# Optimization experiments

Measured on AMD Instinct MI355X. Metric: run time of the kernel, lower is better.

## Reference

```python
import jax, jax.numpy as jnp
import numpy as np

B = 16384   # batch (agents x parallel envs)
IN = 12     # input_dim
H = 64      # hidden_dim -> 2H = 128
OUT = 25    # output_dim (forced by x[:,0:5]..x[:,20:25] slicing)


def setup_inputs() -> dict:
    key = jax.random.key(0)
    ks = jax.random.split(key, 24)
    n = lambda k, s: jax.random.normal(k, s, dtype=jnp.float32)
    s = 0.1  # scale params to keep SiLU/softmax in a sane range
    return {
        "x": n(ks[0], (B, IN)),
        "na": 4,
        # mlp_in: Linear(IN, 2H) + SiLU
        "W_in": n(ks[1], (2 * H, IN)) * s, "b_in": n(ks[2], (2 * H,)) * s,
        # first attention (2H)
        "Aq4": n(ks[3], (2 * H, 2 * H)) * s, "Bq4": n(ks[4], (2 * H,)) * s,
        "Ak4": n(ks[5], (2 * H, 2 * H)) * s, "Bk4": n(ks[6], (2 * H,)) * s,
        "Av4": n(ks[7], (2 * H, 2 * H)) * s, "Bv4": n(ks[8], (2 * H,)) * s,
        # mlp_hidden_4: Linear(2H, H) + SiLU
        "W_h": n(ks[9], (H, 2 * H)) * s, "b_h": n(ks[10], (H,)) * s,
        # second attention (H)
        "Aq7": n(ks[11], (H, H)) * s, "Bq7": n(ks[12], (H,)) * s,
        "Ak7": n(ks[13], (H, H)) * s, "Bk7": n(ks[14], (H,)) * s,
        "Av7": n(ks[15], (H, H)) * s, "Bv7": n(ks[16], (H,)) * s,
        # mlp_out: Linear(H, OUT) + SiLU
        "W_out": n(ks[17], (OUT, H)) * s, "b_out": n(ks[18], (OUT,)) * s,
    }


def _attn(h, Aq, Bq, Ak, Bk, Av, Bv):
    # h: [B, D]; torch does bmm(A, x^T)+B with x of shape [B,1,D] -> seq-len-1
    # attention, i.e. scores are an outer product q k^T of shape [B, D, D].
    q = jax.nn.silu(h @ Aq.T + Bq)                      # [B, D]
    k = jax.nn.silu(h @ Ak.T + Bk)                      # [B, D]
    v = jax.nn.silu(h @ Av.T + Bv)                      # [B, D]
    a = jax.nn.softmax(q[:, :, None] * k[:, None, :], axis=2)  # [B, D, D]
    return jax.nn.silu(jnp.einsum("bij,bj->bi", a, v))  # [B, D]


def reference(x, na, W_in, b_in, Aq4, Bq4, Ak4, Bk4, Av4, Bv4,
              W_h, b_h, Aq7, Bq7, Ak7, Bk7, Av7, Bv7, W_out, b_out):
    h = jax.nn.silu(x @ W_in.T + b_in)                  # [B, 2H]
    h = _attn(h, Aq4, Bq4, Ak4, Bk4, Av4, Bv4)          # [B, 2H]
    h = jax.nn.silu(h @ W_h.T + b_h)                    # [B, H]
    h = _attn(h, Aq7, Bq7, Ak7, Bk7, Av7, Bv7)          # [B, H]
    y = jax.nn.silu(h @ W_out.T + b_out)                # [B, 25]

    # block-diagonal quadratic-form assembly (l=2, kron with ones(1,2))
    M11 = jnp.sum(y[:, 0:5] ** 2, axis=1)               # [B]
    M12 = jnp.sum(y[:, 5:10] ** 2, axis=1)
    M21 = jnp.sum(y[:, 10:15] ** 2, axis=1)
    M22 = jnp.sum(y[:, 15:20] ** 2, axis=1)
    Mpp = jnp.sum(y[:, 20:25] ** 2, axis=1)             # [B]
    q = y[:, :4]                                        # [B, 4] = [q0,q1,q2,q3]
    # M = [[diag(M11), diag(M12)],[diag(M21), diag(M22)]] (each 2x2 diag)
    quad = (M11 * (q[:, 0] ** 2 + q[:, 1] ** 2)
            + (M12 + M21) * (q[:, 0] * q[:, 2] + q[:, 1] * q[:, 3])
            + M22 * (q[:, 2] ** 2 + q[:, 3] ** 2))
    return (quad + Mpp)[:, None]                        # [B, 1]
```

## Files before the change

### kernel.cpp

```cpp
#include <hip/hip_runtime.h>

#define RPW 4
#define WAVES 4
#define RPB (RPW * WAVES)
#define NM 14

using short8 = __attribute__((ext_vector_type(8))) short;
using f32x4  = __attribute__((ext_vector_type(4))) float;

#define LOG2E 1.4426950408889634f

static __device__ __forceinline__ float ex2(float x) { return __builtin_amdgcn_exp2f(x); }
static __device__ __forceinline__ float rcpf_(float x) { return __builtin_amdgcn_rcpf(x); }
static __device__ __forceinline__ float silu_(float x) {
    return x * rcpf_(1.0f + ex2(-x * LOG2E));
}
static __device__ __forceinline__ unsigned short bfhi(float x) {
    return (unsigned short)(__float_as_uint(x) >> 16);
}
static __device__ __forceinline__ unsigned short bfrn(float x) {
    unsigned u = __float_as_uint(x);
    return (unsigned short)((u + 0x7fffu + ((u >> 16) & 1u)) >> 16);
}
static __device__ __forceinline__ float bf2f(unsigned short h) {
    return __uint_as_float(((unsigned)h) << 16);
}

template <int CTRL>
static __device__ __forceinline__ float dpp_rot(float v) {
    return __uint_as_float(
        __builtin_amdgcn_update_dpp(0u, __float_as_uint(v), CTRL, 0xF, 0xF, true));
}
static __device__ __forceinline__ float rsum16(float v) {
    v += dpp_rot<0x128>(v);
    v += dpp_rot<0x124>(v);
    v += dpp_rot<0x122>(v);
    v += dpp_rot<0x121>(v);
    return v;
}

__constant__ float c_invfact[15] = {
    1.f, 1.f, 0.5f, 1.f/6, 1.f/24, 1.f/120, 1.f/720, 1.f/5040, 1.f/40320,
    1.f/362880, 1.f/3628800, 1.f/39916800, 1.f/479001600,
    1.f/6227020800.f, 1.f/87178291200.f};

template <int O, int I>
__device__ __forceinline__ void tr(const float* __restrict__ s, float* __restrict__ d,
                                   int t0, int stride) {
    for (int idx = t0; idx < O * I; idx += stride) {
        int o = idx / I, in = idx - o * I;
        d[in * O + o] = s[idx];
    }
}
template <int N>
__device__ __forceinline__ void cvt(const float* __restrict__ s,
                                    unsigned short* __restrict__ hi,
                                    unsigned short* __restrict__ lo,
                                    int t0, int stride) {
    for (int i = t0; i < N; i += stride) {
        float a = s[i];
        unsigned short h = bfhi(a);
        float r = a - bf2f(h);
        hi[i] = h;
        lo[i] = bfhi(r);
    }
}

__global__ void tweights(const float* __restrict__ s0, const float* __restrict__ s1,
                         const float* __restrict__ s2, const float* __restrict__ s3,
                         const float* __restrict__ s4, const float* __restrict__ s5,
                         const float* __restrict__ s6, const float* __restrict__ s7,
                         const float* __restrict__ s8, float* __restrict__ ws) {
    const int stride = gridDim.x * blockDim.x;
    const int t0 = blockIdx.x * blockDim.x + threadIdx.x;
    tr<128, 12>(s0, ws + 0, t0, stride);
    unsigned short* u4 = (unsigned short*)(ws + 1536);
    cvt<128 * 128>(s1, u4 + 0,     u4 + 16384, t0, stride);
    cvt<128 * 128>(s2, u4 + 32768, u4 + 49152, t0, stride);
    cvt<128 * 128>(s3, u4 + 65536, u4 + 81920, t0, stride);
    unsigned short* wh = (unsigned short*)(ws + 50688);
    cvt<64 * 128>(s4, wh + 0, wh + 8192, t0, stride);
    unsigned short* u7 = (unsigned short*)(ws + 58880);
    cvt<64 * 64>(s5, u7 + 0,     u7 + 4096,  t0, stride);
    cvt<64 * 64>(s6, u7 + 8192,  u7 + 12288, t0, stride);
    cvt<64 * 64>(s7, u7 + 16384, u7 + 20480, t0, stride);
    tr<25, 64>(s8, ws + 71168, t0, stride);
}

__global__ __launch_bounds__(256, 4) void fused_net(
    const float* __restrict__ x, const float* __restrict__ ws,
    const float* __restrict__ b_in,
    const float* __restrict__ Bq4, const float* __restrict__ Bk4, const float* __restrict__ Bv4,
    const float* __restrict__ b_h,
    const float* __restrict__ Bq7, const float* __restrict__ Bk7, const float* __restrict__ Bv7,
    const float* __restrict__ b_out,
    float* __restrict__ out) {
    __shared__ __align__(16) unsigned short hAhi[16][136], hAlo[16][136];
    __shared__ __align__(16) unsigned short h2hi[16][80],  h2lo[16][80];
    __shared__ __align__(16) float sQ[16][132];
    __shared__ __align__(16) unsigned short sKVb[16][132][2];
    __shared__ __align__(16) float h3T[WAVES][64][RPW];
    __shared__ __align__(16) float sXT[WAVES][12][RPW];
    __shared__ __align__(16) float sY[WAVES][RPW][26];

    const int tid = threadIdx.x;
    const int w = tid >> 6;
    const int l = tid & 63;
    const int row0 = blockIdx.x * RPB + w * RPW;
    const int m16 = l & 15, quad = l >> 4;
    const int g = l & 15, r = l >> 4;
    const int R = w * RPW + r;

    const float* WinT  = ws + 0;
    const float* WoutT = ws + 71168;

    if (l < 12 * RPW) {
        float v = x[row0 * 12 + l];
        int rr = l / 12, in = l - rr * 12;
        sXT[w][in][rr] = v;
    }

    {
        float2 bb = *(const float2*)&b_in[2 * l];
        float a0[RPW], a1[RPW];
        #pragma unroll
        for (int rr = 0; rr < RPW; rr++) { a0[rr] = bb.x; a1[rr] = bb.y; }
        #pragma unroll
        for (int in = 0; in < 12; in++) {
            float2 wv = *(const float2*)&WinT[in * 128 + 2 * l];
            float4 xr = *(const float4*)&sXT[w][in][0];
            a0[0] = fmaf(xr.x, wv.x, a0[0]); a1[0] = fmaf(xr.x, wv.y, a1[0]);
            a0[1] = fmaf(xr.y, wv.x, a0[1]); a1[1] = fmaf(xr.y, wv.y, a1[1]);
            a0[2] = fmaf(xr.z, wv.x, a0[2]); a1[2] = fmaf(xr.z, wv.y, a1[2]);
            a0[3] = fmaf(xr.w, wv.x, a0[3]); a1[3] = fmaf(xr.w, wv.y, a1[3]);
        }
        #pragma unroll
        for (int rr = 0; rr < RPW; rr++) {
            float h0 = silu_(a0[rr]), h1 = silu_(a1[rr]);
            unsigned short h0h = bfhi(h0), h1h = bfhi(h1);
            float r0 = h0 - bf2f(h0h), r1 = h1 - bf2f(h1h);
            *(unsigned*)&hAhi[w * 4 + rr][2 * l] = (unsigned)h0h | ((unsigned)h1h << 16);
            *(unsigned*)&hAlo[w * 4 + rr][2 * l] = (unsigned)bfhi(r0) | ((unsigned)bfhi(r1) << 16);
        }
    }
    __syncthreads();

    {
        short8 Ah[4], Al[4];
        #pragma unroll
        for (int kt = 0; kt < 4; kt++) {
            Ah[kt] = *(const short8*)&hAhi[m16][kt * 32 + quad * 8];
            Al[kt] = *(const short8*)&hAlo[m16][kt * 32 + quad * 8];
        }
        const unsigned short* u4 = (const unsigned short*)(ws + 1536);
        #pragma unroll
        for (int t = 0; t < 6; t++) {
            const int nt = w * 6 + t;
            const int mat = nt >> 3;
            const int n = (nt & 7) * 16 + m16;
            const float* bp = (mat == 0) ? Bq4 : (mat == 1) ? Bk4 : Bv4;
            float b = bp[n];
            f32x4 acc = {b, b, b, b};
            const unsigned short* Bh = u4 + mat * 32768 + n * 128;
            const unsigned short* Bl = Bh + 16384;
            #pragma unroll
            for (int kt = 0; kt < 4; kt++) {
                short8 bh = *(const short8*)&Bh[kt * 32 + quad * 8];
                short8 bl = *(const short8*)&Bl[kt * 32 + quad * 8];
                acc = __builtin_amdgcn_mfma_f32_16x16x32_bf16(Ah[kt], bh, acc, 0, 0, 0);
                acc = __builtin_amdgcn_mfma_f32_16x16x32_bf16(Ah[kt], bl, acc, 0, 0, 0);
                acc = __builtin_amdgcn_mfma_f32_16x16x32_bf16(Al[kt], bh, acc, 0, 0, 0);
            }
            #pragma unroll
            for (int reg = 0; reg < 4; reg++) {
                int row = quad * 4 + reg;
                float val = silu_(acc[reg]);
                if (mat == 0)      sQ[row][n] = val;
                else if (mat == 1) sKVb[row][n][0] = bfrn(val);
                else               sKVb[row][n][1] = bfrn(val);
            }
        }
    }
    __syncthreads();

    {
        float dmom[NM];
        float nmom[NM + 1];
        #pragma unroll
        for (int m = 0; m < NM; m++) dmom[m] = 0.f;
        #pragma unroll
        for (int m = 0; m <= NM; m++) nmom[m] = 0.f;
        uint4 u0 = *(const uint4*)&sKVb[R][g * 8][0];
        uint4 u1 = *(const uint4*)&sKVb[R][g * 8 + 4][0];
        unsigned us[8] = {u0.x, u0.y, u0.z, u0.w, u1.x, u1.y, u1.z, u1.w};
        #pragma unroll
        for (int jj = 0; jj < 8; jj++) {
            unsigned u = us[jj];
            float kf = __uint_as_float(u << 16);
            float vf = __uint_as_float(u & 0xffff0000u);
            nmom[0] += vf;
            float p = kf;
            dmom[0] += p; nmom[1] = fmaf(vf, p, nmom[1]);
            #pragma unroll
            for (int m = 1; m < NM; m++) {
                p *= kf;
                dmom[m] += p;
                nmom[m + 1] = fmaf(vf, p, nmom[m + 1]);
            }
        }
        #pragma unroll
        for (int m = 0; m < NM; m++) dmom[m] = rsum16(dmom[m]);
        #pragma unroll
        for (int m = 0; m <= NM; m++) nmom[m] = rsum16(nmom[m]);
        float cd[NM + 1], cn[NM + 1];
        cd[0] = 128.f; cn[0] = nmom[0];
        #pragma unroll
        for (int m = 1; m <= NM; m++) {
            cd[m] = dmom[m - 1] * c_invfact[m];
            cn[m] = nmom[m] * c_invfact[m];
        }
        float4 qa = *(const float4*)&sQ[R][g * 8];
        float4 qb = *(const float4*)&sQ[R][g * 8 + 4];
        float qs[8] = {qa.x, qa.y, qa.z, qa.w, qb.x, qb.y, qb.z, qb.w};
        unsigned hiw[4], low[4];
        #pragma unroll
        for (int i = 0; i < 8; i++) {
            float t = qs[i];
            float d = cd[NM], nn = cn[NM];
            #pragma unroll
            for (int m = NM - 1; m >= 0; m--) {
                d = fmaf(d, t, cd[m]);
                nn = fmaf(nn, t, cn[m]);
            }
            float o = silu_(nn * rcpf_(d));
            unsigned short oh = bfhi(o);
            unsigned short olo = bfhi(o - bf2f(oh));
            if (i & 1) { hiw[i >> 1] |= ((unsigned)oh) << 16; low[i >> 1] |= ((unsigned)olo) << 16; }
            else       { hiw[i >> 1] = oh; low[i >> 1] = olo; }
        }
        *(uint4*)&hAhi[R][g * 8] = make_uint4(hiw[0], hiw[1], hiw[2], hiw[3]);
        *(uint4*)&hAlo[R][g * 8] = make_uint4(low[0], low[1], low[2], low[3]);
    }
    __syncthreads();

    {
        short8 Ah[4], Al[4];
        #pragma unroll
        for (int kt = 0; kt < 4; kt++) {
            Ah[kt] = *(const short8*)&hAhi[m16][kt * 32 + quad * 8];
            Al[kt] = *(const short8*)&hAlo[m16][kt * 32 + quad * 8];
        }
        const unsigned short* whh = (const unsigned short*)(ws + 50688);
        const unsigned short* whl = whh + 8192;
        const int n = w * 16 + m16;
        float b = b_h[n];
        f32x4 acc = {b, b, b, b};
        #pragma unroll
        for (int kt = 0; kt < 4; kt++) {
            short8 bh = *(const short8*)&whh[n * 128 + kt * 32 + quad * 8];
            short8 bl = *(const short8*)&whl[n * 128 + kt * 32 + quad * 8];
            acc = __builtin_amdgcn_mfma_f32_16x16x32_bf16(Ah[kt], bh, acc, 0, 0, 0);
            acc = __builtin_amdgcn_mfma_f32_16x16x32_bf16(Ah[kt], bl, acc, 0, 0, 0);
            acc = __builtin_amdgcn_mfma_f32_16x16x32_bf16(Al[kt], bh, acc, 0, 0, 0);
        }
        #pragma unroll
        for (int reg = 0; reg < 4; reg++) {
            int row = quad * 4 + reg;
            float hv = silu_(acc[reg]);
            unsigned short hh = bfhi(hv);
            h2hi[row][n] = hh;
            h2lo[row][n] = bfhi(hv - bf2f(hh));
        }
    }
    __syncthreads();

    {
        short8 Ah[2], Al[2];
        #pragma unroll
        for (int kt = 0; kt < 2; kt++) {
            Ah[kt] = *(const short8*)&h2hi[m16][kt * 32 + quad * 8];
            Al[kt] = *(const short8*)&h2lo[m16][kt * 32 + quad * 8];
        }
        const unsigned short* u7 = (const unsigned short*)(ws + 58880);
        #pragma unroll
        for (int t = 0; t < 3; t++) {
            const int nt = w * 3 + t;
            const int mat = nt >> 2;
            const int n = (nt & 3) * 16 + m16;
            const float* bp = (mat == 0) ? Bq7 : (mat == 1) ? Bk7 : Bv7;
            float b = bp[n];
            f32x4 acc = {b, b, b, b};
            const unsigned short* Bh = u7 + mat * 8192 + n * 64;
            const unsigned short* Bl = Bh + 4096;
            #pragma unroll
            for (int kt = 0; kt < 2; kt++) {
                short8 bh = *(const short8*)&Bh[kt * 32 + quad * 8];
                short8 bl = *(const short8*)&Bl[kt * 32 + quad * 8];
                acc = __builtin_amdgcn_mfma_f32_16x16x32_bf16(Ah[kt], bh, acc, 0, 0, 0);
                acc = __builtin_amdgcn_mfma_f32_16x16x32_bf16(Ah[kt], bl, acc, 0, 0, 0);
                acc = __builtin_amdgcn_mfma_f32_16x16x32_bf16(Al[kt], bh, acc, 0, 0, 0);
            }
            #pragma unroll
            for (int reg = 0; reg < 4; reg++) {
                int row = quad * 4 + reg;
                float val = silu_(acc[reg]);
                if (mat == 0)      sQ[row][n] = val;
                else if (mat == 1) sKVb[row][n][0] = bfrn(val);
                else               sKVb[row][n][1] = bfrn(val);
            }
        }
    }
    __syncthreads();

    {
        float dmom[NM];
        float nmom[NM + 1];
        #pragma unroll
        for (int m = 0; m < NM; m++) dmom[m] = 0.f;
        #pragma unroll
        for (int m = 0; m <= NM; m++) nmom[m] = 0.f;
        uint4 u0 = *(const uint4*)&sKVb[R][g * 4][0];
        unsigned us[4] = {u0.x, u0.y, u0.z, u0.w};
        #pragma unroll
        for (int jj = 0; jj < 4; jj++) {
            unsigned u = us[jj];
            float kf = __uint_as_float(u << 16);
            float vf = __uint_as_float(u & 0xffff0000u);
            nmom[0] += vf;
            float p = kf;
            dmom[0] += p; nmom[1] = fmaf(vf, p, nmom[1]);
            #pragma unroll
            for (int m = 1; m < NM; m++) {
                p *= kf;
                dmom[m] += p;
                nmom[m + 1] = fmaf(vf, p, nmom[m + 1]);
            }
        }
        #pragma unroll
        for (int m = 0; m < NM; m++) dmom[m] = rsum16(dmom[m]);
        #pragma unroll
        for (int m = 0; m <= NM; m++) nmom[m] = rsum16(nmom[m]);
        float cd[NM + 1], cn[NM + 1];
        cd[0] = 64.f; cn[0] = nmom[0];
        #pragma unroll
        for (int m = 1; m <= NM; m++) {
            cd[m] = dmom[m - 1] * c_invfact[m];
            cn[m] = nmom[m] * c_invfact[m];
        }
        float4 qa = *(const float4*)&sQ[R][g * 4];
        float qs[4] = {qa.x, qa.y, qa.z, qa.w};
        #pragma unroll
        for (int i = 0; i < 4; i++) {
            float t = qs[i];
            float d = cd[NM], nn = cn[NM];
            #pragma unroll
            for (int m = NM - 1; m >= 0; m--) {
                d = fmaf(d, t, cd[m]);
                nn = fmaf(nn, t, cn[m]);
            }
            h3T[w][g * 4 + i][r] = silu_(nn * rcpf_(d));
        }
    }

    {
        const int o = l & 31;
        const int half = l >> 5;
        const int oc = (o < 25) ? o : 0;
        float y[RPW];
        float bb = (half == 0) ? b_out[oc] : 0.f;
        #pragma unroll
        for (int rr = 0; rr < RPW; rr++) y[rr] = bb;
        const int in0 = half * 32;
        #pragma unroll 4
        for (int i = 0; i < 32; i++) {
            int in = in0 + i;
            float wv = WoutT[in * 25 + oc];
            float4 xr = *(const float4*)&h3T[w][in][0];
            y[0] = fmaf(xr.x, wv, y[0]);
            y[1] = fmaf(xr.y, wv, y[1]);
            y[2] = fmaf(xr.z, wv, y[2]);
            y[3] = fmaf(xr.w, wv, y[3]);
        }
        #pragma unroll
        for (int rr = 0; rr < RPW; rr++) {
            float full = y[rr] + __shfl_xor(y[rr], 32, 64);
            if (l < 25) sY[w][rr][l] = silu_(full);
        }
    }

    if (l < RPW) {
        const int rr = l;
        float y[25];
        #pragma unroll
        for (int c = 0; c < 25; c++) y[c] = sY[w][rr][c];
        float M11 = 0.f, M12 = 0.f, M21 = 0.f, M22 = 0.f, Mpp = 0.f;
        #pragma unroll
        for (int c = 0; c < 5; c++) {
            M11 = fmaf(y[c], y[c], M11);
            M12 = fmaf(y[5 + c], y[5 + c], M12);
            M21 = fmaf(y[10 + c], y[10 + c], M21);
            M22 = fmaf(y[15 + c], y[15 + c], M22);
            Mpp = fmaf(y[20 + c], y[20 + c], Mpp);
        }
        float quad = M11 * (y[0] * y[0] + y[1] * y[1])
                   + (M12 + M21) * (y[0] * y[2] + y[1] * y[3])
                   + M22 * (y[2] * y[2] + y[3] * y[3]);
        out[row0 + rr] = quad + Mpp;
    }
}

extern "C" void kernel_launch(void* const* d_in, const int* in_sizes, int n_in,
                              void* d_out, int out_size, void* d_ws, size_t ws_size,
                              hipStream_t stream) {
    const float* x    = (const float*)d_in[0];
    const float* W_in = (const float*)d_in[2];
    const float* b_in = (const float*)d_in[3];
    const float* Aq4  = (const float*)d_in[4];
    const float* Bq4  = (const float*)d_in[5];
    const float* Ak4  = (const float*)d_in[6];
    const float* Bk4  = (const float*)d_in[7];
    const float* Av4  = (const float*)d_in[8];
    const float* Bv4  = (const float*)d_in[9];
    const float* W_h  = (const float*)d_in[10];
    const float* b_h  = (const float*)d_in[11];
    const float* Aq7  = (const float*)d_in[12];
    const float* Bq7  = (const float*)d_in[13];
    const float* Ak7  = (const float*)d_in[14];
    const float* Bk7  = (const float*)d_in[15];
    const float* Av7  = (const float*)d_in[16];
    const float* Bv7  = (const float*)d_in[17];
    const float* Wout = (const float*)d_in[18];
    const float* bout = (const float*)d_in[19];
    float* ws = (float*)d_ws;

    tweights<<<256, 256, 0, stream>>>(W_in, Aq4, Ak4, Av4, W_h, Aq7, Ak7, Av7, Wout, ws);

    const int B = in_sizes[0] / 12;
    const int grid = B / RPB;
    fused_net<<<grid, 256, 0, stream>>>(x, ws, b_in, Bq4, Bk4, Bv4,
                                        b_h, Bq7, Bk7, Bv7, bout, (float*)d_out);
}
```

Measured before the change: 137.1 us.

## Pre-swizzle weights into MFMA fragment order and prefetch B-fragments ahead of use

```diff
diff --git a/kernel.cpp b/kernel.cpp
--- a/kernel.cpp
+++ b/kernel.cpp
@@ -52,17 +52,23 @@
         d[in * O + o] = s[idx];
     }
 }
-template <int N>
-__device__ __forceinline__ void cvt(const float* __restrict__ s,
-                                    unsigned short* __restrict__ hi,
-                                    unsigned short* __restrict__ lo,
-                                    int t0, int stride) {
-    for (int i = t0; i < N; i += stride) {
-        float a = s[i];
-        unsigned short h = bfhi(a);
-        float r = a - bf2f(h);
-        hi[i] = h;
-        lo[i] = bfhi(r);
+
+template <int TILES, int KTS, int K>
+__device__ __forceinline__ void frag_cvt(const float* __restrict__ A,
+                                         unsigned short* __restrict__ dst,
+                                         int t0, int stride) {
+    const int total = TILES * KTS * 2 * 512;
+    for (int idx = t0; idx < total; idx += stride) {
+        int e = idx & 7;
+        int lane = (idx >> 3) & 63;
+        int h = (idx >> 9) & 1;
+        int kt = (idx >> 10) % KTS;
+        int tile = (idx >> 10) / KTS;
+        int row = tile * 16 + (lane & 15);
+        int col = kt * 32 + (lane >> 4) * 8 + e;
+        float a = A[row * K + col];
+        unsigned short hi = bfhi(a);
+        dst[idx] = h ? bfhi(a - bf2f(hi)) : hi;
     }
 }
 
@@ -70,21 +76,20 @@
                          const float* __restrict__ s2, const float* __restrict__ s3,
                          const float* __restrict__ s4, const float* __restrict__ s5,
                          const float* __restrict__ s6, const float* __restrict__ s7,
-                         const float* __restrict__ s8, float* __restrict__ ws) {
+                         float* __restrict__ ws) {
     const int stride = gridDim.x * blockDim.x;
     const int t0 = blockIdx.x * blockDim.x + threadIdx.x;
     tr<128, 12>(s0, ws + 0, t0, stride);
     unsigned short* u4 = (unsigned short*)(ws + 1536);
-    cvt<128 * 128>(s1, u4 + 0,     u4 + 16384, t0, stride);
-    cvt<128 * 128>(s2, u4 + 32768, u4 + 49152, t0, stride);
-    cvt<128 * 128>(s3, u4 + 65536, u4 + 81920, t0, stride);
+    frag_cvt<8, 4, 128>(s1, u4 + 0,     t0, stride);
+    frag_cvt<8, 4, 128>(s2, u4 + 32768, t0, stride);
+    frag_cvt<8, 4, 128>(s3, u4 + 65536, t0, stride);
     unsigned short* wh = (unsigned short*)(ws + 50688);
-    cvt<64 * 128>(s4, wh + 0, wh + 8192, t0, stride);
+    frag_cvt<4, 4, 128>(s4, wh, t0, stride);
     unsigned short* u7 = (unsigned short*)(ws + 58880);
-    cvt<64 * 64>(s5, u7 + 0,     u7 + 4096,  t0, stride);
-    cvt<64 * 64>(s6, u7 + 8192,  u7 + 12288, t0, stride);
-    cvt<64 * 64>(s7, u7 + 16384, u7 + 20480, t0, stride);
-    tr<25, 64>(s8, ws + 71168, t0, stride);
+    frag_cvt<4, 2, 64>(s5, u7 + 0,     t0, stride);
+    frag_cvt<4, 2, 64>(s6, u7 + 8192,  t0, stride);
+    frag_cvt<4, 2, 64>(s7, u7 + 16384, t0, stride);
 }
 
 __global__ __launch_bounds__(256, 4) void fused_net(
@@ -93,7 +98,7 @@
     const float* __restrict__ Bq4, const float* __restrict__ Bk4, const float* __restrict__ Bv4,
     const float* __restrict__ b_h,
     const float* __restrict__ Bq7, const float* __restrict__ Bk7, const float* __restrict__ Bv7,
-    const float* __restrict__ b_out,
+    const float* __restrict__ Wout, const float* __restrict__ b_out,
     float* __restrict__ out) {
     __shared__ __align__(16) unsigned short hAhi[16][136], hAlo[16][136];
     __shared__ __align__(16) unsigned short h2hi[16][80],  h2lo[16][80];
@@ -111,8 +116,27 @@
     const int g = l & 15, r = l >> 4;
     const int R = w * RPW + r;
 
-    const float* WinT  = ws + 0;
-    const float* WoutT = ws + 71168;
+    const float* WinT = ws + 0;
+
+    float bias4[6];
+    #pragma unroll
+    for (int t = 0; t < 6; t++) {
+        const int nt = w * 6 + t;
+        const int mat = nt >> 3;
+        const int n = (nt & 7) * 16 + m16;
+        const float* bp = (mat == 0) ? Bq4 : (mat == 1) ? Bk4 : Bv4;
+        bias4[t] = bp[n];
+    }
+    float biasH = b_h[w * 16 + m16];
+    float bias7[3];
+    #pragma unroll
+    for (int t = 0; t < 3; t++) {
+        const int nt = w * 3 + t;
+        const int mat = nt >> 2;
+        const int n = (nt & 3) * 16 + m16;
+        const float* bp = (mat == 0) ? Bq7 : (mat == 1) ? Bk7 : Bv7;
+        bias7[t] = bp[n];
+    }
 
     if (l < 12 * RPW) {
         float v = x[row0 * 12 + l];
@@ -152,37 +176,57 @@
             Ah[kt] = *(const short8*)&hAhi[m16][kt * 32 + quad * 8];
             Al[kt] = *(const short8*)&hAlo[m16][kt * 32 + quad * 8];
         }
-        const unsigned short* u4 = (const unsigned short*)(ws + 1536);
+        const unsigned short* F4 = (const unsigned short*)(ws + 1536);
+        short8 cb[4][2], nb[4][2];
+        auto ldt = [&](int t, short8 fr[4][2]) {
+            const int nt = w * 6 + t;
+            const int mat = nt >> 3, tile = nt & 7;
+            const unsigned short* bp = F4 + mat * 32768 + tile * 4096 + l * 8;
+            #pragma unroll
+            for (int kt = 0; kt < 4; kt++) {
+                fr[kt][0] = *(const short8*)(bp + kt * 1024);
+                fr[kt][1] = *(const short8*)(bp + kt * 1024 + 512);
+            }
+        };
+        ldt(0, cb);
         #pragma unroll
         for (int t = 0; t < 6; t++) {
+            if (t < 5) ldt(t + 1, nb);
+            f32x4 acc0 = {0.f, 0.f, 0.f, 0.f};
+            f32x4 acc1 = {0.f, 0.f, 0.f, 0.f};
+            #pragma unroll
+            for (int kt = 0; kt < 4; kt++) {
+                acc0 = __builtin_amdgcn_mfma_f32_16x16x32_bf16(Ah[kt], cb[kt][0], acc0, 0, 0, 0);
+                acc1 = __builtin_amdgcn_mfma_f32_16x16x32_bf16(Ah[kt], cb[kt][1], acc1, 0, 0, 0);
+                acc1 = __builtin_amdgcn_mfma_f32_16x16x32_bf16(Al[kt], cb[kt][0], acc1, 0, 0, 0);
+            }
             const int nt = w * 6 + t;
             const int mat = nt >> 3;
             const int n = (nt & 7) * 16 + m16;
-            const float* bp = (mat == 0) ? Bq4 : (mat == 1) ? Bk4 : Bv4;
-            float b = bp[n];
-            f32x4 acc = {b, b, b, b};
-            const unsigned short* Bh = u4 + mat * 32768 + n * 128;
-            const unsigned short* Bl = Bh + 16384;
-            #pragma unroll
-            for (int kt = 0; kt < 4; kt++) {
-                short8 bh = *(const short8*)&Bh[kt * 32 + quad * 8];
-                short8 bl = *(const short8*)&Bl[kt * 32 + quad * 8];
-                acc = __builtin_amdgcn_mfma_f32_16x16x32_bf16(Ah[kt], bh, acc, 0, 0, 0);
-                acc = __builtin_amdgcn_mfma_f32_16x16x32_bf16(Ah[kt], bl, acc, 0, 0, 0);
-                acc = __builtin_amdgcn_mfma_f32_16x16x32_bf16(Al[kt], bh, acc, 0, 0, 0);
-            }
+            const float b = bias4[t];
             #pragma unroll
             for (int reg = 0; reg < 4; reg++) {
                 int row = quad * 4 + reg;
-                float val = silu_(acc[reg]);
+                float val = silu_(b + acc0[reg] + acc1[reg]);
                 if (mat == 0)      sQ[row][n] = val;
                 else if (mat == 1) sKVb[row][n][0] = bfrn(val);
                 else               sKVb[row][n][1] = bfrn(val);
             }
+            #pragma unroll
+            for (int kt = 0; kt < 4; kt++) { cb[kt][0] = nb[kt][0]; cb[kt][1] = nb[kt][1]; }
         }
     }
     __syncthreads();
 
+    short8 whf[4][2];
+    {
+        const unsigned short* bp = (const unsigned short*)(ws + 50688) + w * 4096 + l * 8;
+        #pragma unroll
+        for (int kt = 0; kt < 4; kt++) {
+            whf[kt][0] = *(const short8*)(bp + kt * 1024);
+            whf[kt][1] = *(const short8*)(bp + kt * 1024 + 512);
+        }
+    }
     {
         float dmom[NM];
         float nmom[NM + 1];
@@ -243,6 +287,21 @@
     }
     __syncthreads();
 
+    short8 u7f[3][2][2];
+    {
+        const unsigned short* U7 = (const unsigned short*)(ws + 58880);
+        #pragma unroll
+        for (int t = 0; t < 3; t++) {
+            const int nt = w * 3 + t;
+            const int mat = nt >> 2, tile = nt & 3;
+            const unsigned short* bp = U7 + mat * 8192 + tile * 2048 + l * 8;
+            #pragma unroll
+            for (int kt = 0; kt < 2; kt++) {
+                u7f[t][kt][0] = *(const short8*)(bp + kt * 1024);
+                u7f[t][kt][1] = *(const short8*)(bp + kt * 1024 + 512);
+            }
+        }
+    }
     {
         short8 Ah[4], Al[4];
         #pragma unroll
@@ -250,23 +309,19 @@
             Ah[kt] = *(const short8*)&hAhi[m16][kt * 32 + quad * 8];
             Al[kt] = *(const short8*)&hAlo[m16][kt * 32 + quad * 8];
         }
-        const unsigned short* whh = (const unsigned short*)(ws + 50688);
-        const unsigned short* whl = whh + 8192;
         const int n = w * 16 + m16;
-        float b = b_h[n];
-        f32x4 acc = {b, b, b, b};
+        f32x4 acc0 = {0.f, 0.f, 0.f, 0.f};
+        f32x4 acc1 = {0.f, 0.f, 0.f, 0.f};
         #pragma unroll
         for (int kt = 0; kt < 4; kt++) {
-            short8 bh = *(const short8*)&whh[n * 128 + kt * 32 + quad * 8];
-            short8 bl = *(const short8*)&whl[n * 128 + kt * 32 + quad * 8];
-            acc = __builtin_amdgcn_mfma_f32_16x16x32_bf16(Ah[kt], bh, acc, 0, 0, 0);
-            acc = __builtin_amdgcn_mfma_f32_16x16x32_bf16(Ah[kt], bl, acc, 0, 0, 0);
-            acc = __builtin_amdgcn_mfma_f32_16x16x32_bf16(Al[kt], bh, acc, 0, 0, 0);
+            acc0 = __builtin_amdgcn_mfma_f32_16x16x32_bf16(Ah[kt], whf[kt][0], acc0, 0, 0, 0);
+            acc1 = __builtin_amdgcn_mfma_f32_16x16x32_bf16(Ah[kt], whf[kt][1], acc1, 0, 0, 0);
+            acc1 = __builtin_amdgcn_mfma_f32_16x16x32_bf16(Al[kt], whf[kt][0], acc1, 0, 0, 0);
         }
         #pragma unroll
         for (int reg = 0; reg < 4; reg++) {
             int row = quad * 4 + reg;
-            float hv = silu_(acc[reg]);
+            float hv = silu_(biasH + acc0[reg] + acc1[reg]);
             unsigned short hh = bfhi(hv);
             h2hi[row][n] = hh;
             h2lo[row][n] = bfhi(hv - bf2f(hh));
@@ -281,29 +336,24 @@
             Ah[kt] = *(const short8*)&h2hi[m16][kt * 32 + quad * 8];
             Al[kt] = *(const short8*)&h2lo[m16][kt * 32 + quad * 8];
         }
-        const unsigned short* u7 = (const unsigned short*)(ws + 58880);
         #pragma unroll
         for (int t = 0; t < 3; t++) {
             const int nt = w * 3 + t;
             const int mat = nt >> 2;
             const int n = (nt & 3) * 16 + m16;
-            const float* bp = (mat == 0) ? Bq7 : (mat == 1) ? Bk7 : Bv7;
-            float b = bp[n];
-            f32x4 acc = {b, b, b, b};
-            const unsigned short* Bh = u7 + mat * 8192 + n * 64;
-            const unsigned short* Bl = Bh + 4096;
+            f32x4 acc0 = {0.f, 0.f, 0.f, 0.f};
+            f32x4 acc1 = {0.f, 0.f, 0.f, 0.f};
             #pragma unroll
             for (int kt = 0; kt < 2; kt++) {
-                short8 bh = *(const short8*)&Bh[kt * 32 + quad * 8];
-                short8 bl = *(const short8*)&Bl[kt * 32 + quad * 8];
-                acc = __builtin_amdgcn_mfma_f32_16x16x32_bf16(Ah[kt], bh, acc, 0, 0, 0);
-                acc = __builtin_amdgcn_mfma_f32_16x16x32_bf16(Ah[kt], bl, acc, 0, 0, 0);
-                acc = __builtin_amdgcn_mfma_f32_16x16x32_bf16(Al[kt], bh, acc, 0, 0, 0);
-            }
+                acc0 = __builtin_amdgcn_mfma_f32_16x16x32_bf16(Ah[kt], u7f[t][kt][0], acc0, 0, 0, 0);
+                acc1 = __builtin_amdgcn_mfma_f32_16x16x32_bf16(Ah[kt], u7f[t][kt][1], acc1, 0, 0, 0);
+                acc1 = __builtin_amdgcn_mfma_f32_16x16x32_bf16(Al[kt], u7f[t][kt][0], acc1, 0, 0, 0);
+            }
+            const float b = bias7[t];
             #pragma unroll
             for (int reg = 0; reg < 4; reg++) {
                 int row = quad * 4 + reg;
-                float val = silu_(acc[reg]);
+                float val = silu_(b + acc0[reg] + acc1[reg]);
                 if (mat == 0)      sQ[row][n] = val;
                 else if (mat == 1) sKVb[row][n][0] = bfrn(val);
                 else               sKVb[row][n][1] = bfrn(val);
@@ -312,6 +362,17 @@
     }
     __syncthreads();
 
+    float4 wq[8];
+    float bb7;
+    {
+        const int o_ = l & 31;
+        const int half_ = l >> 5;
+        const int oc_ = (o_ < 25) ? o_ : 0;
+        const float* wp = Wout + oc_ * 64 + half_ * 32;
+        #pragma unroll
+        for (int q = 0; q < 8; q++) wq[q] = *(const float4*)&wp[4 * q];
+        bb7 = (half_ == 0) ? b_out[oc_] : 0.f;
+    }
     {
         float dmom[NM];
         float nmom[NM + 1];
@@ -319,8 +380,9 @@
         for (int m = 0; m < NM; m++) dmom[m] = 0.f;
         #pragma unroll
         for (int m = 0; m <= NM; m++) nmom[m] = 0.f;
-        uint4 u0 = *(const uint4*)&sKVb[R][g * 4][0];
-        unsigned us[4] = {u0.x, u0.y, u0.z, u0.w};
+        uint2 u0 = *(const uint2*)&sKVb[R][g * 4][0];
+        uint2 u1 = *(const uint2*)&sKVb[R][g * 4 + 2][0];
+        unsigned us[4] = {u0.x, u0.y, u1.x, u1.y};
         #pragma unroll
         for (int jj = 0; jj < 4; jj++) {
             unsigned u = us[jj];
@@ -363,23 +425,23 @@
     }
 
     {
-        const int o = l & 31;
         const int half = l >> 5;
-        const int oc = (o < 25) ? o : 0;
         float y[RPW];
-        float bb = (half == 0) ? b_out[oc] : 0.f;
-        #pragma unroll
-        for (int rr = 0; rr < RPW; rr++) y[rr] = bb;
+        #pragma unroll
+        for (int rr = 0; rr < RPW; rr++) y[rr] = bb7;
         const int in0 = half * 32;
-        #pragma unroll 4
-        for (int i = 0; i < 32; i++) {
-            int in = in0 + i;
-            float wv = WoutT[in * 25 + oc];
-            float4 xr = *(const float4*)&h3T[w][in][0];
-            y[0] = fmaf(xr.x, wv, y[0]);
-            y[1] = fmaf(xr.y, wv, y[1]);
-            y[2] = fmaf(xr.z, wv, y[2]);
-            y[3] = fmaf(xr.w, wv, y[3]);
+        #pragma unroll
+        for (int q = 0; q < 8; q++) {
+            float wa[4] = {wq[q].x, wq[q].y, wq[q].z, wq[q].w};
+            #pragma unroll
+            for (int ii = 0; ii < 4; ii++) {
+                int in = in0 + 4 * q + ii;
+                float4 xr = *(const float4*)&h3T[w][in][0];
+                y[0] = fmaf(xr.x, wa[ii], y[0]);
+                y[1] = fmaf(xr.y, wa[ii], y[1]);
+                y[2] = fmaf(xr.z, wa[ii], y[2]);
+                y[3] = fmaf(xr.w, wa[ii], y[3]);
+            }
         }
         #pragma unroll
         for (int rr = 0; rr < RPW; rr++) {
@@ -433,10 +495,10 @@
     const float* bout = (const float*)d_in[19];
     float* ws = (float*)d_ws;
 
-    tweights<<<256, 256, 0, stream>>>(W_in, Aq4, Ak4, Av4, W_h, Aq7, Ak7, Av7, Wout, ws);
+    tweights<<<256, 256, 0, stream>>>(W_in, Aq4, Ak4, Av4, W_h, Aq7, Ak7, Av7, ws);
 
     const int B = in_sizes[0] / 12;
     const int grid = B / RPB;
     fused_net<<<grid, 256, 0, stream>>>(x, ws, b_in, Bq4, Bk4, Bv4,
-                                        b_h, Bq7, Bk7, Bv7, bout, (float*)d_out);
-}
+                                        b_h, Bq7, Bk7, Bv7, Wout, bout, (float*)d_out);
+}
```

Result: faster. 132.6 us (-3.3%).
